# Kernel tuning notes

Hardware: AMD Instinct MI355X
Metric: run time of the kernel (lower is better)

The kernel has to match this reference:

```python
import jax, jax.numpy as jnp
import numpy as np

B, S, H = 2, 256, 768
LR = 0.01
EPS = 1e-5  # torch LayerNorm default


def setup_inputs() -> dict:
    key = jax.random.key(0)
    ks = jax.random.split(key, 6)
    f = jnp.float32
    return {
        "x": jax.random.normal(ks[0], (B, S, H), f),
        "W_init": jax.random.normal(ks[1], (H, H), f) * 0.02,
        "b_init": jnp.zeros((H,), f),
        "gate_w": jax.random.normal(ks[2], (4 * H, H), f) * 0.02,
        "gate_b": jnp.zeros((4 * H,), f),
        "up_w": jax.random.normal(ks[3], (4 * H, H), f) * 0.02,
        "up_b": jnp.zeros((4 * H,), f),
        "down_w": jax.random.normal(ks[4], (H, 4 * H), f) * 0.02,
        "down_b": jnp.zeros((H,), f),
        "norm_w": jnp.ones((H,), f),
        "norm_b": jnp.zeros((H,), f),
    }


def _layernorm(x, w, b):
    mu = jnp.mean(x, axis=-1, keepdims=True)
    var = jnp.var(x, axis=-1, keepdims=True)
    return (x - mu) * jax.lax.rsqrt(var + EPS) * w + b


def reference(x, W_init, b_init, gate_w, gate_b, up_w, up_b,
              down_w, down_b, norm_w, norm_b):
    # x: [B, S, H]. Sequential TTT fast-weight recurrence, vectorized over batch,
    # scanned over time (equivalent to the per-token Python loop in torch).
    Bn, Sn, Hn = x.shape
    xs = jnp.swapaxes(x, 0, 1)                                   # [S, B, H]
    x_next = jnp.concatenate([xs[1:], jnp.zeros_like(xs[:1])], 0)  # target x[t+1]
    # lr per step; the update is skipped at the last token (t == S-1)
    lr = jnp.concatenate([jnp.full((Sn - 1,), LR, x.dtype),
                          jnp.zeros((1,), x.dtype)])

    W0 = jnp.broadcast_to(W_init, (Bn, Hn, Hn))
    b0 = jnp.broadcast_to(b_init, (Bn, Hn))

    def step(carry, inp):
        W, b = carry
        xt, xn, lr_t = inp
        pred = jnp.einsum('bij,bj->bi', W, xt) + b               # fast-weight matvec
        gated = jax.nn.sigmoid(pred @ gate_w.T + gate_b) * (pred @ up_w.T + up_b)
        out = _layernorm(gated @ down_w.T + down_b + pred, norm_w, norm_b)
        diff = pred - xn                                         # prediction error
        W = W - lr_t * diff[:, :, None] * xt[:, None, :]         # rank-1 update
        b = b - lr_t * diff
        return (W, b), out

    _, ys = jax.lax.scan(step, (W0, b0), (xs, x_next, lr))       # ys: [S, B, H]
    return jnp.swapaxes(ys, 0, 1)
```

## Files before the change

### kernel.cpp

```cpp
#include <hip/hip_runtime.h>
#include <hip/hip_bf16.h>

#define H   768
#define H4  3072
#define S   256
#define BB  2
#define M   (BB * S)
#define LRC 0.01f
#define C   64
#define NC  (S / C)

typedef __attribute__((ext_vector_type(8))) short bf16x8;
typedef __attribute__((ext_vector_type(4))) float f32x4;

__device__ inline short bfbits(float f) {
    __hip_bfloat16 h = __float2bfloat16(f);
    return *reinterpret_cast<short*>(&h);
}

__global__ __launch_bounds__(256) void k_stage(
    const float* __restrict__ x,  const float* __restrict__ W0,
    const float* __restrict__ gw, const float* __restrict__ uw,
    const float* __restrict__ dw,
    short* __restrict__ Xhi, short* __restrict__ Xlo,
    short* __restrict__ Whi, short* __restrict__ Wlo,
    short* __restrict__ gw2, short* __restrict__ uw2, short* __restrict__ dw2)
{
    const long gid = (long)blockIdx.x * 256 + threadIdx.x;
    const float* src; short* hp; short* lp = nullptr; long base;
    if (gid < 98304)        { src = x;  hp = Xhi; lp = Xlo; base = 0; }
    else if (gid < 245760)  { src = W0; hp = Whi; lp = Wlo; base = 98304; }
    else if (gid < 835584)  { src = gw; hp = gw2; base = 245760; }
    else if (gid < 1425408) { src = uw; hp = uw2; base = 835584; }
    else                    { src = dw; hp = dw2; base = 1425408; }
    const long i = (gid - base) * 4;
    const float4 v = *(const float4*)(src + i);
    const float vf[4] = {v.x, v.y, v.z, v.w};
    short h4[4], l4[4];
#pragma unroll
    for (int j = 0; j < 4; ++j) {
        h4[j] = bfbits(vf[j]);
        __hip_bfloat16 hb = *reinterpret_cast<__hip_bfloat16*>(&h4[j]);
        l4[j] = bfbits(vf[j] - __bfloat162float(hb));
    }
    *(uint2*)(hp + i) = *(uint2*)h4;
    if (lp) *(uint2*)(lp + i) = *(uint2*)l4;
}

__global__ __launch_bounds__(256) void k_gram_base4(
    const short* __restrict__ Xhi, const short* __restrict__ Xlo,
    const short* __restrict__ Whi, const short* __restrict__ Wlo,
    const float* __restrict__ b0,
    float* __restrict__ g, float* __restrict__ base0, float* __restrict__ U)
{
    __shared__ float Gi[C * 65];
    const int wid = threadIdx.x >> 6, lane = threadIdx.x & 63;
    const int r16 = lane & 15, quad = lane >> 4;
    const int id = blockIdx.x;

    if (id >= 8) {
        const short *Ah, *Al, *Bh, *Bl;
        float bias = 0.f;
        float* outp;
        int outStride, orow0, ocol;
        if (id < 136) {
            const int id2 = id - 8;
            const int b = id2 >> 6;
            const int my = (id2 >> 2) & 15, nx = id2 & 3;
            const int m0 = my * 16, n0 = nx * 64 + wid * 16;
            const short* XH = Xhi + b * S * H;
            const short* XL = Xlo + b * S * H;
            Ah = XH + (m0 + r16) * H;  Al = XL + (m0 + r16) * H;
            Bh = XH + (n0 + r16) * H;  Bl = XL + (n0 + r16) * H;
            bias = 1.f;
            outp = g + (long)(b * S) * S;  outStride = S;
            orow0 = m0; ocol = n0 + r16;
        } else {
            const int id3 = id - 136;
            const int my = id3 / 12, nx = id3 % 12;
            const int m0 = my * 16, n0 = nx * 64 + wid * 16;
            Ah = Xhi + (m0 + r16) * H;  Al = Xlo + (m0 + r16) * H;
            Bh = Whi + (n0 + r16) * H;  Bl = Wlo + (n0 + r16) * H;
            outp = base0;  outStride = H;
            orow0 = m0; ocol = n0 + r16;
            bias = b0[ocol];
        }

        f32x4 acc = (f32x4){0, 0, 0, 0};
        int4 pa[2], pl[2], pb[2], pc[2];
#pragma unroll
        for (int s = 0; s < 2; ++s) {
            const int k = s * 32 + quad * 8;
            pa[s] = *(const int4*)(Ah + k);
            pl[s] = *(const int4*)(Al + k);
            pb[s] = *(const int4*)(Bh + k);
            pc[s] = *(const int4*)(Bl + k);
        }
        for (int it = 0; it < 24; ++it) {
            const int cb = it & 1;
            const bf16x8 ah = *(const bf16x8*)&pa[cb];
            const bf16x8 al = *(const bf16x8*)&pl[cb];
            const bf16x8 bh = *(const bf16x8*)&pb[cb];
            const bf16x8 bl = *(const bf16x8*)&pc[cb];
            if (it + 2 < 24) {
                const int k = (it + 2) * 32 + quad * 8;
                pa[cb] = *(const int4*)(Ah + k);
                pl[cb] = *(const int4*)(Al + k);
                pb[cb] = *(const int4*)(Bh + k);
                pc[cb] = *(const int4*)(Bl + k);
            }
            acc = __builtin_amdgcn_mfma_f32_16x16x32_bf16(ah, bh, acc, 0, 0, 0);
            acc = __builtin_amdgcn_mfma_f32_16x16x32_bf16(ah, bl, acc, 0, 0, 0);
            acc = __builtin_amdgcn_mfma_f32_16x16x32_bf16(al, bh, acc, 0, 0, 0);
        }
#pragma unroll
        for (int r = 0; r < 4; ++r)
            outp[(orow0 + quad * 4 + r) * outStride + ocol] = acc[r] + bias;
    } else {
        const int b = id >> 2, c = id & 3;
        const int t0 = c * C;
        const short* XH = Xhi + (b * S + t0) * H;
        const short* XL = Xlo + (b * S + t0) * H;
        const int m0 = wid * 16;

        f32x4 acc4[4];
#pragma unroll
        for (int j = 0; j < 4; ++j) acc4[j] = (f32x4){0, 0, 0, 0};
        for (int k0 = 0; k0 < H; k0 += 32) {
            const int k = k0 + quad * 8;
            const bf16x8 ah = *(const bf16x8*)(XH + (m0 + r16) * H + k);
            const bf16x8 al = *(const bf16x8*)(XL + (m0 + r16) * H + k);
#pragma unroll
            for (int j = 0; j < 4; ++j) {
                const bf16x8 bh = *(const bf16x8*)(XH + (j * 16 + r16) * H + k);
                const bf16x8 bl = *(const bf16x8*)(XL + (j * 16 + r16) * H + k);
                acc4[j] = __builtin_amdgcn_mfma_f32_16x16x32_bf16(ah, bh, acc4[j], 0, 0, 0);
                acc4[j] = __builtin_amdgcn_mfma_f32_16x16x32_bf16(ah, bl, acc4[j], 0, 0, 0);
                acc4[j] = __builtin_amdgcn_mfma_f32_16x16x32_bf16(al, bh, acc4[j], 0, 0, 0);
            }
        }
#pragma unroll
        for (int j = 0; j < 4; ++j)
#pragma unroll
            for (int r = 0; r < 4; ++r)
                Gi[(m0 + quad * 4 + r) * 65 + j * 16 + r16] = acc4[j][r] + 1.f;
        __syncthreads();

        const int j0 = wid * 16;
        float R[16];
#pragma unroll
        for (int i = 0; i < 16; ++i) R[i] = (lane == j0 + i) ? 1.f : 0.f;
        for (int s = 0; s < C - 1; ++s) {
            const float Gv = Gi[s * 65 + lane];
            const float mlt = (lane > s) ? LRC : 0.f;
#pragma unroll
            for (int i = 0; i < 16; ++i) {
                const float dsb = __shfl(R[i], s, 64);
                R[i] -= mlt * Gv * dsb;
            }
        }
        float* Ub = U + (long)(b * NC + c) * C * C;
#pragma unroll
        for (int i = 0; i < 16; ++i)
            Ub[lane * C + j0 + i] = R[i];
    }
}

__global__ __launch_bounds__(256) void k_recur7(
    const float* __restrict__ x,
    const float* __restrict__ base0,
    const float* __restrict__ g,
    const float* __restrict__ U,
    float* __restrict__ pred_f,
    __hip_bfloat16* __restrict__ pred_h)
{
    __shared__ float  tB[64 * 9];
    __shared__ float  tX[64 * 9];
    __shared__ float2 Dl2[256 * 4];
    __shared__ float2 Rl2[4 * 64];
    __shared__ float  Us[64 * 65];
    __shared__ float  Gslab[192 * 64];
    const int tid = threadIdx.x;
    const int w = tid >> 6, lane = tid & 63;
    const int b = blockIdx.x / 96, hb = blockIdx.x % 96;
    const int h0 = hb * 8;
    const int ho = w * 2;
    const int ct = tid >> 2;
    const int cq = (tid & 3) * 2;

    for (int c = 0; c < NC; ++c) {
        const int t0 = c * C;
        __syncthreads();
        {
            const int gm = b * S + t0 + ct;
            const float2 bv = *(const float2*)(base0 + gm * H + h0 + cq);
            float2 xv = {0.f, 0.f};
            if (t0 + ct + 1 < S)
                xv = *(const float2*)(x + (gm + 1) * H + h0 + cq);
            tB[ct * 9 + cq + 0] = bv.x - xv.x;
            tB[ct * 9 + cq + 1] = bv.y - xv.y;
            tX[ct * 9 + cq + 0] = xv.x;
            tX[ct * 9 + cq + 1] = xv.y;
            const float* Ub = U + (long)(b * NC + c) * C * C;
#pragma unroll
            for (int j = 0; j < 16; ++j) {
                const int idx = tid + 256 * j;
                const int row = idx >> 6, col = idx & 63;
                Us[row * 65 + col] = Ub[row * C + col];
            }
            const float* gb = g + (long)(b * S) * S + t0;
            for (int i = tid; i < t0 * 64; i += 256) {
                const int row = i >> 6, col = i & 63;
                Gslab[i] = gb[(long)row * S + col];
            }
        }
        __syncthreads();
        float R[2], Xn[2];
#pragma unroll
        for (int h = 0; h < 2; ++h) {
            R[h]  = tB[lane * 9 + ho + h];
            Xn[h] = tX[lane * 9 + ho + h];
        }
#pragma unroll 8
        for (int cs = 0; cs < t0; ++cs) {
            const float Gv = Gslab[cs * 64 + lane];
            const float2 dr = Dl2[cs * 4 + w];
            R[0] -= LRC * Gv * dr.x;
            R[1] -= LRC * Gv * dr.y;
        }
        Rl2[w * 64 + lane] = (float2){R[0], R[1]};
        float D[2] = {0.f, 0.f};
#pragma unroll 8
        for (int s = 0; s < C; ++s) {
            const float2 rb = Rl2[w * 64 + s];
            const float uv = Us[lane * 65 + s];
            D[0] += uv * rb.x;
            D[1] += uv * rb.y;
        }
        Dl2[(t0 + lane) * 4 + w] = (float2){D[0], D[1]};
        __syncthreads();
#pragma unroll
        for (int h = 0; h < 2; ++h) tB[lane * 9 + ho + h] = D[h] + Xn[h];
        __syncthreads();
        {
            const int gm = b * S + t0 + ct;
            float2 pv;
            pv.x = tB[ct * 9 + cq + 0];
            pv.y = tB[ct * 9 + cq + 1];
            *(float2*)(pred_f + gm * H + h0 + cq) = pv;
            short p2[2];
            p2[0] = bfbits(pv.x); p2[1] = bfbits(pv.y);
            *(unsigned int*)((short*)pred_h + gm * H + h0 + cq) = *(unsigned int*)p2;
        }
    }
}

#define RS 40
__global__ __launch_bounds__(256) void k_gateup4(
    const __hip_bfloat16* __restrict__ predh,
    const short* __restrict__ gwp, const float* __restrict__ gb,
    const short* __restrict__ uwp, const float* __restrict__ ub,
    __hip_bfloat16* __restrict__ hid)
{
    __shared__ int4 smv[960];
    short* sm = (short*)smv;
    short* sA = sm;
    short* sG = sm + 64 * RS;
    short* sU = sm + 128 * RS;

    const int tid = threadIdx.x;
    const int wid = tid >> 6, lane = tid & 63;
    const int r16 = lane & 15, quad = lane >> 4;
    const int wm = wid & 1, wn = (wid >> 1) & 1;
    const int n0 = blockIdx.x * 64;
    const int m0 = blockIdx.y * 64;

    const int srow = tid >> 2;
    const int sch  = (tid & 3) * 8;
    const short* A = (const short*)predh;

    f32x4 ag[2][2], au[2][2];
#pragma unroll
    for (int i = 0; i < 2; ++i)
#pragma unroll
        for (int j = 0; j < 2; ++j) { ag[i][j] = (f32x4){0,0,0,0}; au[i][j] = (f32x4){0,0,0,0}; }

    int4 rA, rG, rU;
    rA = *(const int4*)(A   + (m0 + srow) * H + sch);
    rG = *(const int4*)(gwp + (n0 + srow) * H + sch);
    rU = *(const int4*)(uwp + (n0 + srow) * H + sch);
    for (int it = 0; it < 24; ++it) {
        *(int4*)(sA + srow * RS + sch) = rA;
        *(int4*)(sG + srow * RS + sch) = rG;
        *(int4*)(sU + srow * RS + sch) = rU;
        __syncthreads();
        if (it < 23) {
            const int k = (it + 1) * 32 + sch;
            rA = *(const int4*)(A   + (m0 + srow) * H + k);
            rG = *(const int4*)(gwp + (n0 + srow) * H + k);
            rU = *(const int4*)(uwp + (n0 + srow) * H + k);
        }
        bf16x8 aF[2], gF[2], uF[2];
#pragma unroll
        for (int i = 0; i < 2; ++i) {
            aF[i] = *(const bf16x8*)(sA + (wm * 32 + i * 16 + r16) * RS + quad * 8);
            gF[i] = *(const bf16x8*)(sG + (wn * 32 + i * 16 + r16) * RS + quad * 8);
            uF[i] = *(const bf16x8*)(sU + (wn * 32 + i * 16 + r16) * RS + quad * 8);
        }
#pragma unroll
        for (int i = 0; i < 2; ++i)
#pragma unroll
            for (int j = 0; j < 2; ++j) {
                ag[i][j] = __builtin_amdgcn_mfma_f32_16x16x32_bf16(aF[i], gF[j], ag[i][j], 0, 0, 0);
                au[i][j] = __builtin_amdgcn_mfma_f32_16x16x32_bf16(aF[i], uF[j], au[i][j], 0, 0, 0);
            }
        __syncthreads();
    }
#pragma unroll
    for (int j = 0; j < 2; ++j) {
        const int ocol = n0 + wn * 32 + j * 16 + r16;
        const float gbv = gb[ocol], ubv = ub[ocol];
#pragma unroll
        for (int i = 0; i < 2; ++i)
#pragma unroll
            for (int r = 0; r < 4; ++r) {
                const int orow = m0 + wm * 32 + i * 16 + quad * 4 + r;
                const float gg = ag[i][j][r] + gbv;
                const float u  = au[i][j][r] + ubv;
                const float sg = 1.f / (1.f + __expf(-gg));
                hid[orow * H4 + ocol] = __float2bfloat16(sg * u);
            }
    }
}

__device__ inline bf16x8 ldb16(const void* p, long off) {
    return *(const bf16x8*)((const short*)p + off);
}
__global__ __launch_bounds__(256) void k_down4(
    const __hip_bfloat16* __restrict__ hid,
    const short* __restrict__ dwp,
    float* __restrict__ dpart)
{
    const int wid = threadIdx.x >> 6, lane = threadIdx.x & 63;
    const int r16 = lane & 15, quad = lane >> 4;
    const int m0 = blockIdx.y * 32;
    const int n0 = blockIdx.x * 64 + wid * 16;
    const int kz = blockIdx.z;

    f32x4 ac[2];
    ac[0] = (f32x4){0,0,0,0}; ac[1] = (f32x4){0,0,0,0};
    const short* A = (const short*)hid;
    const long brow = (long)(n0 + r16) * H4;

    const int kbeg = kz * 768, kend = kbeg + 768;
    for (int k0 = kbeg; k0 < kend; k0 += 32) {
        const int k = k0 + quad * 8;
        const bf16x8 bd = ldb16(dwp, brow + k);
#pragma unroll
        for (int i = 0; i < 2; ++i) {
            const bf16x8 af = *(const bf16x8*)(A + (m0 + i * 16 + r16) * H4 + k);
            ac[i] = __builtin_amdgcn_mfma_f32_16x16x32_bf16(af, bd, ac[i], 0, 0, 0);
        }
    }
    float* dp = dpart + (long)kz * M * H;
    const int ocol = n0 + r16;
#pragma unroll
    for (int i = 0; i < 2; ++i)
#pragma unroll
        for (int r = 0; r < 4; ++r) {
            const int orow = m0 + i * 16 + quad * 4 + r;
            dp[orow * H + ocol] = ac[i][r];
        }
}

__global__ __launch_bounds__(256) void k_ln2(
    const float* __restrict__ dpart,
    const float* __restrict__ db,
    const float* __restrict__ predf,
    const float* __restrict__ nw,
    const float* __restrict__ nb,
    float* __restrict__ out)
{
    const int m = blockIdx.x;
    const int tid = threadIdx.x;

    float v[3];
    float s = 0.f, s2 = 0.f;
#pragma unroll
    for (int j = 0; j < 3; ++j) {
        const int hh = tid + 256 * j;
        const long o = (long)m * H + hh;
        float t = dpart[o] + dpart[o + (long)M * H]
                + dpart[o + 2L * M * H] + dpart[o + 3L * M * H]
                + db[hh] + predf[o];
        v[j] = t;
        s += t;
        s2 += t * t;
    }
#pragma unroll
    for (int off = 32; off >= 1; off >>= 1) {
        s  += __shfl_xor(s, off, 64);
        s2 += __shfl_xor(s2, off, 64);
    }
    __shared__ float rs[4], rs2[4];
    const int wid = tid >> 6, lane = tid & 63;
    if (lane == 0) { rs[wid] = s; rs2[wid] = s2; }
    __syncthreads();
    s  = rs[0] + rs[1] + rs[2] + rs[3];
    s2 = rs2[0] + rs2[1] + rs2[2] + rs2[3];
    const float mu  = s / (float)H;
    const float var = s2 / (float)H - mu * mu;
    const float inv = rsqrtf(var + 1e-5f);
#pragma unroll
    for (int j = 0; j < 3; ++j) {
        const int hh = tid + 256 * j;
        out[m * H + hh] = (v[j] - mu) * inv * nw[hh] + nb[hh];
    }
}

extern "C" void kernel_launch(void* const* d_in, const int* in_sizes, int n_in,
                              void* d_out, int out_size, void* d_ws, size_t ws_size,
                              hipStream_t stream)
{
    const float* x   = (const float*)d_in[0];
    const float* W0  = (const float*)d_in[1];
    const float* b0  = (const float*)d_in[2];
    const float* gw  = (const float*)d_in[3];
    const float* gb  = (const float*)d_in[4];
    const float* uw  = (const float*)d_in[5];
    const float* ub  = (const float*)d_in[6];
    const float* dw  = (const float*)d_in[7];
    const float* db  = (const float*)d_in[8];
    const float* nw  = (const float*)d_in[9];
    const float* nb  = (const float*)d_in[10];

    char* ws = (char*)d_ws;
    float*          pred_f = (float*)(ws);
    __hip_bfloat16* pred_h = (__hip_bfloat16*)(ws + 1572864);
    __hip_bfloat16* hid    = (__hip_bfloat16*)(ws + 2359296);
    float*          base0  = (float*)(ws + 5505024);
    float*          g      = (float*)(ws + 7077888);
    short*          Xhi    = (short*)(ws + 7602176);
    short*          Xlo    = (short*)(ws + 8388608);
    short*          Whi    = (short*)(ws + 9175040);
    short*          Wlo    = (short*)(ws + 10354688);
    float*          U      = (float*)(ws + 11534336);
    short* gw2 = (short*)(ws + 11665408);
    short* uw2 = (short*)(ws + 11665408 + 4718592);
    short* dw2 = (short*)(ws + 11665408 + 2 * 4718592);
    float* dpart = (float*)(ws + 25821184);

    k_stage<<<dim3(2015232 / 256), 256, 0, stream>>>(
        x, W0, gw, uw, dw, Xhi, Xlo, Whi, Wlo, gw2, uw2, dw2);
    k_gram_base4<<<dim3(520), 256, 0, stream>>>(Xhi, Xlo, Whi, Wlo, b0, g, base0, U);
    k_recur7<<<dim3(192), 256, 0, stream>>>(x, base0, g, U, pred_f, pred_h);
    k_gateup4<<<dim3(H4 / 64, M / 64), 256, 0, stream>>>(pred_h, gw2, gb, uw2, ub, hid);
    k_down4<<<dim3(H / 64, M / 32, 4), 256, 0, stream>>>(hid, dw2, dpart);
    k_ln2<<<dim3(M), 256, 0, stream>>>(dpart, db, pred_f, nw, nb, (float*)d_out);
}
```

Measured before the change: 219.0 us.

## Split chunk-inverse into separate kernel and widen gram/base tiles to 32 rows

The combined gram/base kernel used to run 8 special blocks that recomputed the 64x64 diagonal Gram blocks and did the triangular solve, alongside 512 blocks of 16-row tiles. Now the GEMM kernel uses 32-row tiles (two MFMA accumulators sharing B loads) over 256 blocks, and a new small kernel reads the diagonal blocks of g and runs the triangular solve. This removes the long serial tail from the GEMM launch and improves operand reuse. In exchange it adds a kernel launch and a dependency, and the solve now waits for the whole GEMM to finish.

```diff
diff --git a/kernel.cpp b/kernel.cpp
--- a/kernel.cpp
+++ b/kernel.cpp
@@ -47,123 +47,122 @@
     if (lp) *(uint2*)(lp + i) = *(uint2*)l4;
 }
 
-__global__ __launch_bounds__(256) void k_gram_base4(
+__global__ __launch_bounds__(256) void k_gram_base5(
     const short* __restrict__ Xhi, const short* __restrict__ Xlo,
     const short* __restrict__ Whi, const short* __restrict__ Wlo,
     const float* __restrict__ b0,
-    float* __restrict__ g, float* __restrict__ base0, float* __restrict__ U)
-{
-    __shared__ float Gi[C * 65];
+    float* __restrict__ g, float* __restrict__ base0)
+{
     const int wid = threadIdx.x >> 6, lane = threadIdx.x & 63;
     const int r16 = lane & 15, quad = lane >> 4;
     const int id = blockIdx.x;
 
-    if (id >= 8) {
-        const short *Ah, *Al, *Bh, *Bl;
-        float bias = 0.f;
-        float* outp;
-        int outStride, orow0, ocol;
-        if (id < 136) {
-            const int id2 = id - 8;
-            const int b = id2 >> 6;
-            const int my = (id2 >> 2) & 15, nx = id2 & 3;
-            const int m0 = my * 16, n0 = nx * 64 + wid * 16;
-            const short* XH = Xhi + b * S * H;
-            const short* XL = Xlo + b * S * H;
-            Ah = XH + (m0 + r16) * H;  Al = XL + (m0 + r16) * H;
-            Bh = XH + (n0 + r16) * H;  Bl = XL + (n0 + r16) * H;
-            bias = 1.f;
-            outp = g + (long)(b * S) * S;  outStride = S;
-            orow0 = m0; ocol = n0 + r16;
-        } else {
-            const int id3 = id - 136;
-            const int my = id3 / 12, nx = id3 % 12;
-            const int m0 = my * 16, n0 = nx * 64 + wid * 16;
-            Ah = Xhi + (m0 + r16) * H;  Al = Xlo + (m0 + r16) * H;
-            Bh = Whi + (n0 + r16) * H;  Bl = Wlo + (n0 + r16) * H;
-            outp = base0;  outStride = H;
-            orow0 = m0; ocol = n0 + r16;
-            bias = b0[ocol];
-        }
-
-        f32x4 acc = (f32x4){0, 0, 0, 0};
-        int4 pa[2], pl[2], pb[2], pc[2];
-#pragma unroll
-        for (int s = 0; s < 2; ++s) {
-            const int k = s * 32 + quad * 8;
-            pa[s] = *(const int4*)(Ah + k);
-            pl[s] = *(const int4*)(Al + k);
-            pb[s] = *(const int4*)(Bh + k);
-            pc[s] = *(const int4*)(Bl + k);
-        }
-        for (int it = 0; it < 24; ++it) {
-            const int cb = it & 1;
-            const bf16x8 ah = *(const bf16x8*)&pa[cb];
-            const bf16x8 al = *(const bf16x8*)&pl[cb];
-            const bf16x8 bh = *(const bf16x8*)&pb[cb];
-            const bf16x8 bl = *(const bf16x8*)&pc[cb];
-            if (it + 2 < 24) {
-                const int k = (it + 2) * 32 + quad * 8;
-                pa[cb] = *(const int4*)(Ah + k);
-                pl[cb] = *(const int4*)(Al + k);
-                pb[cb] = *(const int4*)(Bh + k);
-                pc[cb] = *(const int4*)(Bl + k);
-            }
-            acc = __builtin_amdgcn_mfma_f32_16x16x32_bf16(ah, bh, acc, 0, 0, 0);
-            acc = __builtin_amdgcn_mfma_f32_16x16x32_bf16(ah, bl, acc, 0, 0, 0);
-            acc = __builtin_amdgcn_mfma_f32_16x16x32_bf16(al, bh, acc, 0, 0, 0);
-        }
+    const short *A0h, *A0l, *A1h, *A1l, *Bh, *Bl;
+    float bias = 0.f;
+    float* outp;
+    int outStride, orow0, ocol;
+    if (id < 64) {
+        const int bx = id & 3, by = (id >> 2) & 7, b = id >> 5;
+        const int m0 = by * 32, n0 = bx * 64 + wid * 16;
+        const short* XH = Xhi + b * S * H;
+        const short* XL = Xlo + b * S * H;
+        A0h = XH + (m0 + r16) * H;       A0l = XL + (m0 + r16) * H;
+        A1h = XH + (m0 + 16 + r16) * H;  A1l = XL + (m0 + 16 + r16) * H;
+        Bh  = XH + (n0 + r16) * H;       Bl  = XL + (n0 + r16) * H;
+        bias = 1.f;
+        outp = g + (long)(b * S) * S;  outStride = S;
+        orow0 = m0; ocol = n0 + r16;
+    } else {
+        const int id2 = id - 64;
+        const int m0 = (id2 / 12) * 32, n0 = (id2 % 12) * 64 + wid * 16;
+        A0h = Xhi + (m0 + r16) * H;       A0l = Xlo + (m0 + r16) * H;
+        A1h = Xhi + (m0 + 16 + r16) * H;  A1l = Xlo + (m0 + 16 + r16) * H;
+        Bh  = Whi + (n0 + r16) * H;       Bl  = Wlo + (n0 + r16) * H;
+        outp = base0;  outStride = H;
+        orow0 = m0; ocol = n0 + r16;
+        bias = b0[ocol];
+    }
+
+    f32x4 acc[2];
+    acc[0] = (f32x4){0, 0, 0, 0};
+    acc[1] = (f32x4){0, 0, 0, 0};
+    int4 pa0[2], pl0[2], pa1[2], pl1[2], pb[2], pc[2];
+#pragma unroll
+    for (int s = 0; s < 2; ++s) {
+        const int k = s * 32 + quad * 8;
+        pa0[s] = *(const int4*)(A0h + k);
+        pl0[s] = *(const int4*)(A0l + k);
+        pa1[s] = *(const int4*)(A1h + k);
+        pl1[s] = *(const int4*)(A1l + k);
+        pb[s]  = *(const int4*)(Bh + k);
+        pc[s]  = *(const int4*)(Bl + k);
+    }
+    for (int it = 0; it < 24; ++it) {
+        const int cb = it & 1;
+        const bf16x8 a0h = *(const bf16x8*)&pa0[cb];
+        const bf16x8 a0l = *(const bf16x8*)&pl0[cb];
+        const bf16x8 a1h = *(const bf16x8*)&pa1[cb];
+        const bf16x8 a1l = *(const bf16x8*)&pl1[cb];
+        const bf16x8 bh  = *(const bf16x8*)&pb[cb];
+        const bf16x8 bl  = *(const bf16x8*)&pc[cb];
+        if (it + 2 < 24) {
+            const int k = (it + 2) * 32 + quad * 8;
+            pa0[cb] = *(const int4*)(A0h + k);
+            pl0[cb] = *(const int4*)(A0l + k);
+            pa1[cb] = *(const int4*)(A1h + k);
+            pl1[cb] = *(const int4*)(A1l + k);
+            pb[cb]  = *(const int4*)(Bh + k);
+            pc[cb]  = *(const int4*)(Bl + k);
+        }
+        acc[0] = __builtin_amdgcn_mfma_f32_16x16x32_bf16(a0h, bh, acc[0], 0, 0, 0);
+        acc[0] = __builtin_amdgcn_mfma_f32_16x16x32_bf16(a0h, bl, acc[0], 0, 0, 0);
+        acc[0] = __builtin_amdgcn_mfma_f32_16x16x32_bf16(a0l, bh, acc[0], 0, 0, 0);
+        acc[1] = __builtin_amdgcn_mfma_f32_16x16x32_bf16(a1h, bh, acc[1], 0, 0, 0);
+        acc[1] = __builtin_amdgcn_mfma_f32_16x16x32_bf16(a1h, bl, acc[1], 0, 0, 0);
+        acc[1] = __builtin_amdgcn_mfma_f32_16x16x32_bf16(a1l, bh, acc[1], 0, 0, 0);
+    }
+#pragma unroll
+    for (int i = 0; i < 2; ++i)
 #pragma unroll
         for (int r = 0; r < 4; ++r)
-            outp[(orow0 + quad * 4 + r) * outStride + ocol] = acc[r] + bias;
-    } else {
-        const int b = id >> 2, c = id & 3;
-        const int t0 = c * C;
-        const short* XH = Xhi + (b * S + t0) * H;
-        const short* XL = Xlo + (b * S + t0) * H;
-        const int m0 = wid * 16;
-
-        f32x4 acc4[4];
-#pragma unroll
-        for (int j = 0; j < 4; ++j) acc4[j] = (f32x4){0, 0, 0, 0};
-        for (int k0 = 0; k0 < H; k0 += 32) {
-            const int k = k0 + quad * 8;
-            const bf16x8 ah = *(const bf16x8*)(XH + (m0 + r16) * H + k);
-            const bf16x8 al = *(const bf16x8*)(XL + (m0 + r16) * H + k);
-#pragma unroll
-            for (int j = 0; j < 4; ++j) {
-                const bf16x8 bh = *(const bf16x8*)(XH + (j * 16 + r16) * H + k);
-                const bf16x8 bl = *(const bf16x8*)(XL + (j * 16 + r16) * H + k);
-                acc4[j] = __builtin_amdgcn_mfma_f32_16x16x32_bf16(ah, bh, acc4[j], 0, 0, 0);
-                acc4[j] = __builtin_amdgcn_mfma_f32_16x16x32_bf16(ah, bl, acc4[j], 0, 0, 0);
-                acc4[j] = __builtin_amdgcn_mfma_f32_16x16x32_bf16(al, bh, acc4[j], 0, 0, 0);
-            }
-        }
-#pragma unroll
-        for (int j = 0; j < 4; ++j)
-#pragma unroll
-            for (int r = 0; r < 4; ++r)
-                Gi[(m0 + quad * 4 + r) * 65 + j * 16 + r16] = acc4[j][r] + 1.f;
-        __syncthreads();
-
-        const int j0 = wid * 16;
-        float R[16];
-#pragma unroll
-        for (int i = 0; i < 16; ++i) R[i] = (lane == j0 + i) ? 1.f : 0.f;
-        for (int s = 0; s < C - 1; ++s) {
-            const float Gv = Gi[s * 65 + lane];
-            const float mlt = (lane > s) ? LRC : 0.f;
-#pragma unroll
-            for (int i = 0; i < 16; ++i) {
-                const float dsb = __shfl(R[i], s, 64);
-                R[i] -= mlt * Gv * dsb;
-            }
-        }
-        float* Ub = U + (long)(b * NC + c) * C * C;
-#pragma unroll
-        for (int i = 0; i < 16; ++i)
-            Ub[lane * C + j0 + i] = R[i];
-    }
+            outp[(orow0 + i * 16 + quad * 4 + r) * outStride + ocol] = acc[i][r] + bias;
+}
+
+__global__ __launch_bounds__(256) void k_inv(
+    const float* __restrict__ g, float* __restrict__ U)
+{
+    __shared__ float Gi[C * 65];
+    const int tid = threadIdx.x;
+    const int w = tid >> 6, lane = tid & 63;
+    const int b = blockIdx.x >> 2, c = blockIdx.x & 3;
+    const int t0 = c * C;
+
+#pragma unroll
+    for (int j = 0; j < 16; ++j) {
+        const int idx = tid + 256 * j;
+        const int row = idx >> 6, col = idx & 63;
+        Gi[row * 65 + col] = g[(long)(b * S + t0 + row) * S + t0 + col];
+    }
+    __syncthreads();
+
+    const int j0 = w * 16;
+    float R[16];
+#pragma unroll
+    for (int i = 0; i < 16; ++i) R[i] = (lane == j0 + i) ? 1.f : 0.f;
+
+    for (int s = 0; s < C - 1; ++s) {
+        const float Gv = Gi[s * 65 + lane];
+        const float mlt = (lane > s) ? LRC : 0.f;
+#pragma unroll
+        for (int i = 0; i < 16; ++i) {
+            const float dsb = __shfl(R[i], s, 64);
+            R[i] -= mlt * Gv * dsb;
+        }
+    }
+    float* Ub = U + (long)(b * NC + c) * C * C;
+#pragma unroll
+    for (int i = 0; i < 16; ++i)
+        Ub[lane * C + j0 + i] = R[i];
 }
 
 __global__ __launch_bounds__(256) void k_recur7(
@@ -452,7 +451,8 @@
 
     k_stage<<<dim3(2015232 / 256), 256, 0, stream>>>(
         x, W0, gw, uw, dw, Xhi, Xlo, Whi, Wlo, gw2, uw2, dw2);
-    k_gram_base4<<<dim3(520), 256, 0, stream>>>(Xhi, Xlo, Whi, Wlo, b0, g, base0, U);
+    k_gram_base5<<<dim3(256), 256, 0, stream>>>(Xhi, Xlo, Whi, Wlo, b0, g, base0);
+    k_inv<<<dim3(BB * NC), 256, 0, stream>>>(g, U);
     k_recur7<<<dim3(192), 256, 0, stream>>>(x, base0, g, U, pred_f, pred_h);
     k_gateup4<<<dim3(H4 / 64, M / 64), 256, 0, stream>>>(pred_h, gw2, gb, uw2, ub, hid);
     k_down4<<<dim3(H / 64, M / 32, 4), 256, 0, stream>>>(hid, dw2, dpart);
```

Result: faster. 188.6 us (-13.9%).
